# Kernel optimization log

Hardware: AMD Instinct MI355X
Metric: run time of the kernel (lower is better)

## Reference

```python
import jax, jax.numpy as jnp
import numpy as np

BINS = 70
HLO, HHI = -10.0, 10.0
EPS = 1e-5


def _conv_bn(x, w, b, g, be, relu=True):
    # 1x1 Conv1d == channel matmul: x [B,C,N], w [O,C]
    y = jnp.einsum('oc,bcn->bon', w, x) + b[None, :, None]
    # BatchNorm1d in training mode: biased batch stats over (batch, points)
    m = jnp.mean(y, axis=(0, 2))
    v = jnp.var(y, axis=(0, 2))
    y = (y - m[None, :, None]) * jax.lax.rsqrt(v + EPS)[None, :, None]
    y = y * g[None, :, None] + be[None, :, None]
    return jax.nn.relu(y) if relu else y


def _batch_hist(x):
    # Faithful to the torch.histc global-offset hack: one flat histogram with
    # bins*B*F buckets and group offsets of exactly (HHI-HLO); values that fall
    # outside [HLO,HHI] for a given (b,f) leak into neighboring groups, exactly
    # as in the original. Returns argmax bin index per (b,f) as float.
    B, F, N = x.shape
    w = (HHI - HLO) / BINS  # 2/7, and group offset 20 == BINS*w so bins align
    total = BINS * B * F
    grp = jnp.arange(B * F, dtype=jnp.int32).reshape(B, F, 1)
    gidx = jnp.floor((x - HLO) / w).astype(jnp.int32) + BINS * grp
    gidx = jnp.where((gidx >= 0) & (gidx < total), gidx, total)  # drop out-of-range
    counts = jnp.zeros(total + 1, jnp.float32).at[gidx.ravel()].add(1.0)
    h = counts[:total].reshape(B, F, BINS)
    return jnp.argmax(h, axis=-1).astype(jnp.float32)  # [B,F]


def setup_inputs() -> dict:
    key = jax.random.key(0)
    ks = jax.random.split(key, 7)
    d = {
        'x': jax.random.normal(ks[0], (16, 3, 4096), dtype=jnp.float32),
        'w1': jax.random.normal(ks[1], (64, 3), dtype=jnp.float32) * 0.2,
        'b1': jnp.zeros((64,), jnp.float32),
        'g1': jnp.ones((64,), jnp.float32),
        'be1': jnp.zeros((64,), jnp.float32),
        'w2': jax.random.normal(ks[2], (128, 64), dtype=jnp.float32) * 0.1,
        'b2': jnp.zeros((128,), jnp.float32),
        'g2': jnp.ones((128,), jnp.float32),
        'be2': jnp.zeros((128,), jnp.float32),
        'w3': jax.random.normal(ks[3], (1024, 128), dtype=jnp.float32) * 0.08,
        'b3': jnp.zeros((1024,), jnp.float32),
        'g3': jnp.ones((1024,), jnp.float32),
        'be3': jnp.zeros((1024,), jnp.float32),
    }
    return d


def reference(x, w1, b1, g1, be1, w2, b2, g2, be2, w3, b3, g3, be3):
    # PointNetEncoder forward, global_feat=True, robust_type='HS',
    # input/feature transforms disabled (trans, trans_feat are None).
    h = _conv_bn(x, w1, b1, g1, be1, relu=True)    # [B,64,N]
    h = _conv_bn(h, w2, b2, g2, be2, relu=True)    # [B,128,N]
    h = _conv_bn(h, w3, b3, g3, be3, relu=False)   # [B,1024,N]
    feat = _batch_hist(h)                          # [B,1024] mode-bin indices
    return feat
```

## Files before the change

### kernel.cpp

```cpp
#include <hip/hip_runtime.h>

#define EPSF 1e-5f
#define TOTBINS 1146880

typedef _Float16 v8h __attribute__((ext_vector_type(8)));
typedef _Float16 v4h __attribute__((ext_vector_type(4)));
typedef float v4f __attribute__((ext_vector_type(4)));

#define OFF_PARTX   1146880
#define OFF_W1F     1149952
#define OFF_B1F     1150144
#define OFF_PMU1    1150208
#define OFF_M1N     1166592
#define OFF_MU1     1170688
#define OFF_W2H     1170752
#define OFF_W2L     1174848
#define OFF_B2F     1178944
#define OFF_PMU2    1179072
#define OFF_M2N     1211840
#define OFF_MU2     1228224
#define OFF_W3H     1228352
#define OFF_W3L     1293888
#define OFF_B3F     1359424
#define OFF_H1H     1360448
#define OFF_H1L     3457600
#define OFF_H2H     5554752
#define OFF_H2L     9749056

#define GLL(src,dst) __builtin_amdgcn_global_load_lds( \
    (const __attribute__((address_space(1))) void*)(src), \
    (__attribute__((address_space(3))) void*)(dst), 16, 0, 0)

__global__ void k_statsX(const float* __restrict__ x, float* __restrict__ part){
  __shared__ float red[12][256];
  int t = threadIdx.x;
  int s = blockIdx.x*256 + t;
  int b = s >> 12, n = s & 4095;
  const float* xb = x + (size_t)b*12288 + n;
  float x0 = xb[0], x1 = xb[4096], x2 = xb[8192];
  float v[12] = {x0,x1,x2, x0*x0,x0*x1,x0*x2, x1*x1,x1*x2,x2*x2, 0.f,0.f,0.f};
  #pragma unroll
  for(int j=0;j<12;j++) red[j][t]=v[j];
  __syncthreads();
  for(int off=128; off>0; off>>=1){
    if(t<off){
      #pragma unroll
      for(int j=0;j<12;j++) red[j][t]+=red[j][t+off];
    }
    __syncthreads();
  }
  if(t<12) part[blockIdx.x*12+t]=red[t][0];
}

__global__ void k_fold1(const float* __restrict__ part,
                        const float* __restrict__ w1, const float* __restrict__ b1,
                        const float* __restrict__ g1, const float* __restrict__ be1,
                        float* __restrict__ W1f, float* __restrict__ B1f){
  __shared__ double S[12];
  int t=threadIdx.x;
  if(t<12){
    double a=0.0;
    for(int s=0;s<256;s++) a+=(double)part[s*12+t];
    S[t]=a;
  }
  __syncthreads();
  if(t<64){
    double inv = 1.0/65536.0;
    double mu[3]={S[0]*inv,S[1]*inv,S[2]*inv};
    double M[3][3];
    M[0][0]=S[3]*inv; M[0][1]=S[4]*inv; M[0][2]=S[5]*inv;
    M[1][1]=S[6]*inv; M[1][2]=S[7]*inv; M[2][2]=S[8]*inv;
    M[1][0]=M[0][1]; M[2][0]=M[0][2]; M[2][1]=M[1][2];
    double w[3]={(double)w1[t*3],(double)w1[t*3+1],(double)w1[t*3+2]};
    double wm=0.0, q=0.0;
    for(int c=0;c<3;c++){
      wm += w[c]*mu[c];
      for(int d=0;d<3;d++) q += w[c]*w[d]*M[c][d];
    }
    double var = q - wm*wm;
    double m = wm + (double)b1[t];
    double sc = (double)g1[t] / sqrt(var + (double)EPSF);
    for(int c=0;c<3;c++) W1f[t*3+c]=(float)(w[c]*sc);
    B1f[t]=(float)(((double)b1[t]-m)*sc + (double)be1[t]);
  }
}

__global__ void k_layer1(const float* __restrict__ x, const float* __restrict__ W1f,
                         const float* __restrict__ B1f,
                         _Float16* __restrict__ h1h, _Float16* __restrict__ h1l){
  int s = blockIdx.x*256 + threadIdx.x;
  int b = s>>12, n = s&4095;
  const float* xb = x + (size_t)b*12288 + n;
  float x0=xb[0], x1=xb[4096], x2=xb[8192];
  size_t off = ((size_t)((b<<12)+n))<<6;
  #pragma unroll
  for(int q=0;q<8;q++){
    v8h vh, vl;
    #pragma unroll
    for(int e=0;e<8;e++){
      int f=q*8+e;
      float v = fmaf(W1f[f*3+2],x2, fmaf(W1f[f*3+1],x1, fmaf(W1f[f*3],x0, B1f[f])));
      v = v>0.f ? v : 0.f;
      _Float16 hh=(_Float16)v;
      vh[e]=hh;
      vl[e]=(_Float16)(v-(float)hh);
    }
    *(v8h*)(h1h+off+q*8)=vh;
    *(v8h*)(h1l+off+q*8)=vl;
  }
}

__global__ void k_stats1(const _Float16* __restrict__ h1h, const _Float16* __restrict__ h1l,
                         float* __restrict__ partM, float* __restrict__ partMu){
  __shared__ __align__(16) float tl[64][68];
  int t=threadIdx.x, wg=blockIdx.x;
  int s0=wg*256;
  int b=s0>>12, n0=s0&4095;
  int ti=t&15, tj=t>>4;
  float acc[4][4];
  #pragma unroll
  for(int i=0;i<4;i++){
    #pragma unroll
    for(int j=0;j<4;j++) acc[i][j]=0.f;
  }
  float mu=0.f;
  for(int tile=0; tile<4; tile++){
    int nb=n0+tile*64;
    __syncthreads();
    {
      int nr=t>>2, cq=(t&3)<<4;
      const _Float16* ph = h1h + (((size_t)((b<<12)+nb+nr))<<6) + cq;
      const _Float16* pl = h1l + (((size_t)((b<<12)+nb+nr))<<6) + cq;
      #pragma unroll
      for(int q=0;q<2;q++){
        v8h hh=*(const v8h*)(ph+q*8);
        v8h ll=*(const v8h*)(pl+q*8);
        float4 v0=make_float4((float)hh[0]+(float)ll[0],(float)hh[1]+(float)ll[1],
                              (float)hh[2]+(float)ll[2],(float)hh[3]+(float)ll[3]);
        float4 v1=make_float4((float)hh[4]+(float)ll[4],(float)hh[5]+(float)ll[5],
                              (float)hh[6]+(float)ll[6],(float)hh[7]+(float)ll[7]);
        *(float4*)&tl[nr][cq+q*8]   = v0;
        *(float4*)&tl[nr][cq+q*8+4] = v1;
      }
    }
    __syncthreads();
    for(int k=0;k<64;k++){
      float a[4],bb[4];
      #pragma unroll
      for(int i=0;i<4;i++) a[i]=tl[k][i*16+ti];
      #pragma unroll
      for(int j=0;j<4;j++) bb[j]=tl[k][j*16+tj];
      #pragma unroll
      for(int i=0;i<4;i++){
        #pragma unroll
        for(int j=0;j<4;j++) acc[i][j]=fmaf(a[i],bb[j],acc[i][j]);
      }
    }
    if(t<64){
      float ss=0.f;
      for(int k=0;k<64;k++) ss+=tl[k][t];
      mu+=ss;
    }
  }
  #pragma unroll
  for(int i=0;i<4;i++){
    #pragma unroll
    for(int j=0;j<4;j++)
      partM[(size_t)wg*4096+(i*16+ti)*64+(j*16+tj)]=acc[i][j];
  }
  if(t<64) partMu[wg*64+t]=mu;
}

__global__ void k_reduceM1(const float* __restrict__ partM, const float* __restrict__ partMu,
                           float* __restrict__ M1n, float* __restrict__ mu1){
  int e=blockIdx.x*256+threadIdx.x;
  double a=0.0;
  for(int s=0;s<256;s++) a+=(double)partM[(size_t)s*4096+e];
  M1n[e]=(float)(a/65536.0);
  if(e<64){
    double m=0.0;
    for(int s=0;s<256;s++) m+=(double)partMu[s*64+e];
    mu1[e]=(float)(m/65536.0);
  }
}

__global__ void k_fold2(const float* __restrict__ w2, const float* __restrict__ b2,
                        const float* __restrict__ g2, const float* __restrict__ be2,
                        const float* __restrict__ M1n, const float* __restrict__ mu1,
                        _Float16* __restrict__ w2h, _Float16* __restrict__ w2l,
                        float* __restrict__ B2f){
  int f=blockIdx.x, t=threadIdx.x;
  __shared__ float w[64];
  w[t]=w2[f*64+t];
  __syncthreads();
  double tm=0.0;
  for(int c=0;c<64;c++) tm += (double)w[c]*(double)M1n[c*64+t];
  double pv=tm*(double)w[t];
  double pm=(double)w[t]*(double)mu1[t];
  #pragma unroll
  for(int off=32;off>0;off>>=1){
    pv+=__shfl_xor(pv,off,64);
    pm+=__shfl_xor(pm,off,64);
  }
  double var=pv-pm*pm;
  double m=pm+(double)b2[f];
  double sc=(double)g2[f]/sqrt(var+(double)EPSF);
  float Wf=(float)((double)w[t]*sc);
  _Float16 hh=(_Float16)Wf;
  w2h[f*64+t]=hh;
  w2l[f*64+t]=(_Float16)(Wf-(float)hh);
  if(t==0) B2f[f]=(float)(((double)b2[f]-m)*sc+(double)be2[f]);
}

__global__ __launch_bounds__(256,8) void k_layer2(
    const _Float16* __restrict__ h1h, const _Float16* __restrict__ h1l,
    const _Float16* __restrict__ w2h, const _Float16* __restrict__ w2l,
    const float* __restrict__ B2f,
    _Float16* __restrict__ h2h, _Float16* __restrict__ h2l){
  __shared__ __align__(16) _Float16 stage[4][512];
  int t=threadIdx.x, wg=blockIdx.x;
  int wv=t>>6, l=t&63;
  int lrow=l&15, lgrp=l>>4;
  int b=wg>>7;
  int r=wg&127;
  int f0=(r>>6)<<6;
  int n0=(r&63)<<6;
  v8h Ah[2], Al[2];
  {
    const _Float16* ph = w2h + (size_t)(f0 + wv*16 + lrow)*64 + lgrp*8;
    const _Float16* pl = w2l + (size_t)(f0 + wv*16 + lrow)*64 + lgrp*8;
    #pragma unroll
    for(int s=0;s<2;s++){
      Ah[s]=*(const v8h*)(ph+s*32);
      Al[s]=*(const v8h*)(pl+s*32);
    }
  }
  float bias[4];
  #pragma unroll
  for(int rr=0;rr<4;rr++) bias[rr]=B2f[f0+wv*16+lgrp*4+rr];
  int ks=wv>>1, pln=wv&1;
  const _Float16* src = (pln ? h1l : h1h)
      + (((size_t)((b<<12)+n0+lrow))<<6) + ks*32 + lgrp*8;
  _Float16* dst = &stage[wv][0];
  for(int it=0; it<4; it++){
    GLL(src,dst);
    src += 1024;
    __syncthreads();
    v8h Bh[2],Bl[2];
    #pragma unroll
    for(int s=0;s<2;s++){
      Bh[s]=*(const v8h*)&stage[s*2  ][l*8];
      Bl[s]=*(const v8h*)&stage[s*2+1][l*8];
    }
    v4f acc={bias[0],bias[1],bias[2],bias[3]};
    #pragma unroll
    for(int s=0;s<2;s++){
      acc=__builtin_amdgcn_mfma_f32_16x16x32_f16(Ah[s],Bh[s],acc,0,0,0);
      acc=__builtin_amdgcn_mfma_f32_16x16x32_f16(Ah[s],Bl[s],acc,0,0,0);
      acc=__builtin_amdgcn_mfma_f32_16x16x32_f16(Al[s],Bh[s],acc,0,0,0);
    }
    int n=n0+it*16+lrow;
    size_t o=(((size_t)((b<<12)+n))<<7) + f0 + wv*16 + lgrp*4;
    v4h sh, sl4;
    #pragma unroll
    for(int rr=0;rr<4;rr++){
      float v=acc[rr];
      v = v>0.f ? v : 0.f;
      _Float16 hh=(_Float16)v;
      sh[rr]=hh;
      sl4[rr]=(_Float16)(v-(float)hh);
    }
    *(v4h*)(h2h+o)=sh;
    *(v4h*)(h2l+o)=sl4;
    __syncthreads();
  }
}

__global__ void k_stats2(const _Float16* __restrict__ h2h, const _Float16* __restrict__ h2l,
                         float* __restrict__ partM, float* __restrict__ partMu){
  __shared__ __align__(16) float tl[64][132];
  int t=threadIdx.x, wg=blockIdx.x;
  int s0=wg*256;
  int b=s0>>12, n0=s0&4095;
  int ti=t&15, tj=t>>4;
  float acc[8][8];
  #pragma unroll
  for(int i=0;i<8;i++){
    #pragma unroll
    for(int j=0;j<8;j++) acc[i][j]=0.f;
  }
  float mu=0.f;
  for(int tile=0; tile<4; tile++){
    int nb=n0+tile*64;
    __syncthreads();
    {
      int nr=t>>2, cq=(t&3)<<5;
      const _Float16* ph = h2h + ((size_t)((b<<12)+nb+nr))*128 + cq;
      const _Float16* pl = h2l + ((size_t)((b<<12)+nb+nr))*128 + cq;
      #pragma unroll
      for(int q=0;q<4;q++){
        v8h hh=*(const v8h*)(ph+q*8);
        v8h ll=*(const v8h*)(pl+q*8);
        float4 v0=make_float4((float)hh[0]+(float)ll[0],(float)hh[1]+(float)ll[1],
                              (float)hh[2]+(float)ll[2],(float)hh[3]+(float)ll[3]);
        float4 v1=make_float4((float)hh[4]+(float)ll[4],(float)hh[5]+(float)ll[5],
                              (float)hh[6]+(float)ll[6],(float)hh[7]+(float)ll[7]);
        *(float4*)&tl[nr][cq+q*8]   = v0;
        *(float4*)&tl[nr][cq+q*8+4] = v1;
      }
    }
    __syncthreads();
    for(int k=0;k<64;k++){
      float a[8],bb[8];
      #pragma unroll
      for(int i=0;i<8;i++) a[i]=tl[k][i*16+ti];
      #pragma unroll
      for(int j=0;j<8;j++) bb[j]=tl[k][j*16+tj];
      #pragma unroll
      for(int i=0;i<8;i++){
        #pragma unroll
        for(int j=0;j<8;j++) acc[i][j]=fmaf(a[i],bb[j],acc[i][j]);
      }
    }
    if(t<128){
      float s=0.f;
      for(int k=0;k<64;k++) s+=tl[k][t];
      mu+=s;
    }
  }
  #pragma unroll
  for(int i=0;i<8;i++){
    #pragma unroll
    for(int j=0;j<8;j++)
      partM[(size_t)wg*16384+(i*16+ti)*128+(j*16+tj)]=acc[i][j];
  }
  if(t<128) partMu[wg*128+t]=mu;
}

__global__ void k_reduceM2(const float* __restrict__ partM, const float* __restrict__ partMu,
                           float* __restrict__ M2n, float* __restrict__ mu2){
  int e=blockIdx.x*256+threadIdx.x;
  double a=0.0;
  for(int s=0;s<256;s++) a+=(double)partM[(size_t)s*16384+e];
  M2n[e]=(float)(a/65536.0);
  if(e<128){
    double m=0.0;
    for(int s=0;s<256;s++) m+=(double)partMu[s*128+e];
    mu2[e]=(float)(m/65536.0);
  }
}

__global__ void k_fold3(const float* __restrict__ w3, const float* __restrict__ b3,
                        const float* __restrict__ g3, const float* __restrict__ be3,
                        const float* __restrict__ M2n, const float* __restrict__ mu2,
                        _Float16* __restrict__ w3h, _Float16* __restrict__ w3l,
                        float* __restrict__ B3f){
  int f=blockIdx.x, t=threadIdx.x;
  __shared__ float w[128];
  __shared__ double rv[2], rm[2];
  w[t]=w3[f*128+t];
  __syncthreads();
  double tm=0.0;
  for(int c=0;c<128;c++) tm += (double)w[c]*(double)M2n[c*128+t];
  double pv=tm*(double)w[t];
  double pm=(double)w[t]*(double)mu2[t];
  #pragma unroll
  for(int off=32;off>0;off>>=1){
    pv+=__shfl_xor(pv,off,64);
    pm+=__shfl_xor(pm,off,64);
  }
  if((t&63)==0){ rv[t>>6]=pv; rm[t>>6]=pm; }
  __syncthreads();
  double pmt=rm[0]+rm[1];
  double var=(rv[0]+rv[1]) - pmt*pmt;
  double m=pmt + (double)b3[f];
  double sc=(double)g3[f]/sqrt(var+(double)EPSF);
  float Wf=(float)((double)w[t]*sc);
  _Float16 hh=(_Float16)Wf;
  w3h[f*128+t]=hh;
  w3l[f*128+t]=(_Float16)(Wf-(float)hh);
  if(t==0) B3f[f]=(float)(((double)b3[f]-m)*sc+(double)be3[f]);
}

__global__ __launch_bounds__(256,4) void k_gemm3_hist(
    const _Float16* __restrict__ h2h, const _Float16* __restrict__ h2l,
    const _Float16* __restrict__ w3h, const _Float16* __restrict__ w3l,
    const float* __restrict__ B3f, unsigned int* __restrict__ hist){
  __shared__ __align__(16) _Float16 stage[2][8][512];
  __shared__ unsigned int lh[4480];
  int t=threadIdx.x, wg=blockIdx.x;
  int wv=t>>6, l=t&63;
  int lrow=l&15, lgrp=l>>4;
  int b=wg>>6;
  int r=wg&63;
  int f0=(r>>3)<<7;
  int sl=r&7;
  int base=70*((b<<10)+f0);
  for(int i=t;i<4480;i+=256) lh[i]=0u;

  v8h Ah[2][4], Al[2][4];
  #pragma unroll
  for(int T=0;T<2;T++){
    const _Float16* ph = w3h + (size_t)(f0 + wv*32 + T*16 + lrow)*128 + lgrp*8;
    const _Float16* pl = w3l + (size_t)(f0 + wv*32 + T*16 + lrow)*128 + lgrp*8;
    #pragma unroll
    for(int s=0;s<4;s++){
      Ah[T][s]=*(const v8h*)(ph+s*32);
      Al[T][s]=*(const v8h*)(pl+s*32);
    }
  }
  float bias[2][4]; int base70[2][4];
  #pragma unroll
  for(int T=0;T<2;T++){
    #pragma unroll
    for(int rr=0;rr<4;rr++){
      int fl_=wv*32+T*16+lgrp*4+rr;
      bias[T][rr]=B3f[f0+fl_];
      base70[T][rr]=fl_*70;
    }
  }
  const float wbin=(10.0f-(-10.0f))/70.0f;
  const float inv_w=1.0f/wbin;
  const float off_w=10.0f*inv_w;

  const _Float16* pH = h2h + ((size_t)((b<<12)+sl*512+lrow))*128 + wv*32 + lgrp*8;
  const _Float16* pL = h2l + ((size_t)((b<<12)+sl*512+lrow))*128 + wv*32 + lgrp*8;

#define ISSUE(B_) { GLL(pH,&stage[B_][wv*2][0]); GLL(pL,&stage[B_][wv*2+1][0]); \
                    pH+=2048; pL+=2048; }
#define COMPUTE(B_) { \
    v4f acc0={bias[0][0],bias[0][1],bias[0][2],bias[0][3]}; \
    v4f acc1={bias[1][0],bias[1][1],bias[1][2],bias[1][3]}; \
    _Pragma("unroll") \
    for(int s=0;s<4;s++){ \
      v8h Bh=*(const v8h*)&stage[B_][s*2  ][l*8]; \
      v8h Bl=*(const v8h*)&stage[B_][s*2+1][l*8]; \
      acc0=__builtin_amdgcn_mfma_f32_16x16x32_f16(Ah[0][s],Bh,acc0,0,0,0); \
      acc0=__builtin_amdgcn_mfma_f32_16x16x32_f16(Ah[0][s],Bl,acc0,0,0,0); \
      acc0=__builtin_amdgcn_mfma_f32_16x16x32_f16(Al[0][s],Bh,acc0,0,0,0); \
      acc1=__builtin_amdgcn_mfma_f32_16x16x32_f16(Ah[1][s],Bh,acc1,0,0,0); \
      acc1=__builtin_amdgcn_mfma_f32_16x16x32_f16(Ah[1][s],Bl,acc1,0,0,0); \
      acc1=__builtin_amdgcn_mfma_f32_16x16x32_f16(Al[1][s],Bh,acc1,0,0,0); \
    } \
    _Pragma("unroll") \
    for(int T=0;T<2;T++){ \
      v4f accT = T ? acc1 : acc0; \
      _Pragma("unroll") \
      for(int rr=0;rr<4;rr++){ \
        float q=fmaf(accT[rr],inv_w,off_w); \
        if(q>-2.0e9f && q<2.0e9f){ \
          int bin=(int)floorf(q); \
          int loc=base70[T][rr]+bin; \
          if((unsigned)loc<8960u){ \
            atomicAdd(&lh[loc>>1], 1u<<((loc&1)<<4)); \
          }else{ \
            int g=base+loc; \
            if(g>=0 && g<TOTBINS) atomicAdd(&hist[g],1u); \
          } \
        } \
      } \
    } }

  ISSUE(0);
  __syncthreads();
  for(int ii=0;ii<16;ii++){
    ISSUE(1);
    COMPUTE(0);
    __syncthreads();
    if(ii<15) ISSUE(0);
    COMPUTE(1);
    __syncthreads();
  }
#undef ISSUE
#undef COMPUTE
  for(int i=t;i<4480;i+=256){
    unsigned int c=lh[i];
    if(c&0xFFFFu) atomicAdd(&hist[base+2*i],   c&0xFFFFu);
    if(c>>16)     atomicAdd(&hist[base+2*i+1], c>>16);
  }
}

__global__ void k_argmax(const unsigned int* __restrict__ hist, float* __restrict__ out){
  int g = blockIdx.x*256 + threadIdx.x;
  const unsigned int* h = hist + (size_t)g*70;
  unsigned int best=h[0]; int arg=0;
  for(int k=1;k<70;k++){
    unsigned int c=h[k];
    if(c>best){ best=c; arg=k; }
  }
  out[g]=(float)arg;
}

extern "C" void kernel_launch(void* const* d_in, const int* in_sizes, int n_in,
                              void* d_out, int out_size, void* d_ws, size_t ws_size,
                              hipStream_t stream){
  const float* x  =(const float*)d_in[0];
  const float* w1 =(const float*)d_in[1];
  const float* b1 =(const float*)d_in[2];
  const float* g1 =(const float*)d_in[3];
  const float* be1=(const float*)d_in[4];
  const float* w2 =(const float*)d_in[5];
  const float* b2 =(const float*)d_in[6];
  const float* g2 =(const float*)d_in[7];
  const float* be2=(const float*)d_in[8];
  const float* w3 =(const float*)d_in[9];
  const float* b3 =(const float*)d_in[10];
  const float* g3 =(const float*)d_in[11];
  const float* be3=(const float*)d_in[12];

  float* ws=(float*)d_ws;
  unsigned int* hist=(unsigned int*)ws;
  float* partX = ws+OFF_PARTX;
  float* W1f   = ws+OFF_W1F;
  float* B1f   = ws+OFF_B1F;
  float* pMu1  = ws+OFF_PMU1;
  float* M1n   = ws+OFF_M1N;
  float* mu1   = ws+OFF_MU1;
  _Float16* w2h=(_Float16*)(ws+OFF_W2H);
  _Float16* w2l=(_Float16*)(ws+OFF_W2L);
  float* B2f   = ws+OFF_B2F;
  float* pMu2  = ws+OFF_PMU2;
  float* M2n   = ws+OFF_M2N;
  float* mu2   = ws+OFF_MU2;
  _Float16* w3h=(_Float16*)(ws+OFF_W3H);
  _Float16* w3l=(_Float16*)(ws+OFF_W3L);
  float* B3f   = ws+OFF_B3F;
  _Float16* h1h=(_Float16*)(ws+OFF_H1H);
  _Float16* h1l=(_Float16*)(ws+OFF_H1L);
  _Float16* h2h=(_Float16*)(ws+OFF_H2H);
  _Float16* h2l=(_Float16*)(ws+OFF_H2L);
  float* partM1=(float*)(ws+OFF_H2H);
  float* partM2=(float*)(ws+OFF_H1H);

  hipMemsetAsync(hist, 0, (size_t)TOTBINS*sizeof(unsigned int), stream);

  k_statsX  <<<256,256,0,stream>>>(x, partX);
  k_fold1   <<<1,  256,0,stream>>>(partX,w1,b1,g1,be1,W1f,B1f);
  k_layer1  <<<256,256,0,stream>>>(x,W1f,B1f,h1h,h1l);
  k_stats1  <<<256,256,0,stream>>>(h1h,h1l,partM1,pMu1);
  k_reduceM1<<<16, 256,0,stream>>>(partM1,pMu1,M1n,mu1);
  k_fold2   <<<128, 64,0,stream>>>(w2,b2,g2,be2,M1n,mu1,w2h,w2l,B2f);
  k_layer2  <<<2048,256,0,stream>>>(h1h,h1l,w2h,w2l,B2f,h2h,h2l);
  k_stats2  <<<256,256,0,stream>>>(h2h,h2l,partM2,pMu2);
  k_reduceM2<<<64, 256,0,stream>>>(partM2,pMu2,M2n,mu2);
  k_fold3   <<<1024,128,0,stream>>>(w3,b3,g3,be3,M2n,mu2,w3h,w3l,B3f);
  k_gemm3_hist<<<1024,256,0,stream>>>(h2h,h2l,w3h,w3l,B3f,hist);
  k_argmax  <<<64, 256,0,stream>>>(hist,(float*)d_out);
}
```

Baseline: 251.5 us.

## Privatize layer-3 LDS histogram into four 8-bit copies; double-buffer layer-2 staging

The fused GEMM3+histogram kernel now keeps four private LDS histogram copies selected by lane&3. Each copy packs four 8-bit counters per word instead of two 16-bit counters, which should cut LDS atomic contention. The copies are summed when flushed to global memory. The fused kernel's launch bounds drop from 4 to 3 blocks per CU to make room for the larger LDS footprint. Layer 2 gets a double-buffered stage so the next global-to-LDS load overlaps the current MFMA compute. The NaN/huge-value range check before the float-to-int conversion is removed, and the 8-bit counters depend on per-copy counts staying at or below 255.

```diff
diff --git a/kernel.cpp b/kernel.cpp
--- a/kernel.cpp
+++ b/kernel.cpp
@@ -217,7 +217,7 @@
     const _Float16* __restrict__ w2h, const _Float16* __restrict__ w2l,
     const float* __restrict__ B2f,
     _Float16* __restrict__ h2h, _Float16* __restrict__ h2l){
-  __shared__ __align__(16) _Float16 stage[4][512];
+  __shared__ __align__(16) _Float16 stage[2][4][512];
   int t=threadIdx.x, wg=blockIdx.x;
   int wv=t>>6, l=t&63;
   int lrow=l&15, lgrp=l>>4;
@@ -241,39 +241,44 @@
   int ks=wv>>1, pln=wv&1;
   const _Float16* src = (pln ? h1l : h1h)
       + (((size_t)((b<<12)+n0+lrow))<<6) + ks*32 + lgrp*8;
-  _Float16* dst = &stage[wv][0];
-  for(int it=0; it<4; it++){
-    GLL(src,dst);
-    src += 1024;
-    __syncthreads();
-    v8h Bh[2],Bl[2];
-    #pragma unroll
-    for(int s=0;s<2;s++){
-      Bh[s]=*(const v8h*)&stage[s*2  ][l*8];
-      Bl[s]=*(const v8h*)&stage[s*2+1][l*8];
-    }
-    v4f acc={bias[0],bias[1],bias[2],bias[3]};
-    #pragma unroll
-    for(int s=0;s<2;s++){
-      acc=__builtin_amdgcn_mfma_f32_16x16x32_f16(Ah[s],Bh[s],acc,0,0,0);
-      acc=__builtin_amdgcn_mfma_f32_16x16x32_f16(Ah[s],Bl[s],acc,0,0,0);
-      acc=__builtin_amdgcn_mfma_f32_16x16x32_f16(Al[s],Bh[s],acc,0,0,0);
-    }
-    int n=n0+it*16+lrow;
-    size_t o=(((size_t)((b<<12)+n))<<7) + f0 + wv*16 + lgrp*4;
-    v4h sh, sl4;
-    #pragma unroll
-    for(int rr=0;rr<4;rr++){
-      float v=acc[rr];
-      v = v>0.f ? v : 0.f;
-      _Float16 hh=(_Float16)v;
-      sh[rr]=hh;
-      sl4[rr]=(_Float16)(v-(float)hh);
-    }
-    *(v4h*)(h2h+o)=sh;
-    *(v4h*)(h2l+o)=sl4;
-    __syncthreads();
-  }
+
+#define L2ISSUE(B_) { GLL(src,&stage[B_][wv][0]); src += 1024; }
+#define L2COMPUTE(B_,IT) { \
+    v8h Bh[2],Bl[2]; \
+    _Pragma("unroll") \
+    for(int s=0;s<2;s++){ \
+      Bh[s]=*(const v8h*)&stage[B_][s*2  ][l*8]; \
+      Bl[s]=*(const v8h*)&stage[B_][s*2+1][l*8]; \
+    } \
+    v4f acc={bias[0],bias[1],bias[2],bias[3]}; \
+    _Pragma("unroll") \
+    for(int s=0;s<2;s++){ \
+      acc=__builtin_amdgcn_mfma_f32_16x16x32_f16(Ah[s],Bh[s],acc,0,0,0); \
+      acc=__builtin_amdgcn_mfma_f32_16x16x32_f16(Ah[s],Bl[s],acc,0,0,0); \
+      acc=__builtin_amdgcn_mfma_f32_16x16x32_f16(Al[s],Bh[s],acc,0,0,0); \
+    } \
+    int n=n0+(IT)*16+lrow; \
+    size_t o=(((size_t)((b<<12)+n))<<7) + f0 + wv*16 + lgrp*4; \
+    v4h sh, sl4; \
+    _Pragma("unroll") \
+    for(int rr=0;rr<4;rr++){ \
+      float v=acc[rr]; \
+      v = v>0.f ? v : 0.f; \
+      _Float16 hh=(_Float16)v; \
+      sh[rr]=hh; \
+      sl4[rr]=(_Float16)(v-(float)hh); \
+    } \
+    *(v4h*)(h2h+o)=sh; \
+    *(v4h*)(h2l+o)=sl4; }
+
+  L2ISSUE(0);
+  __syncthreads();
+  L2ISSUE(1); L2COMPUTE(0,0); __syncthreads();
+  L2ISSUE(0); L2COMPUTE(1,1); __syncthreads();
+  L2ISSUE(1); L2COMPUTE(0,2); __syncthreads();
+              L2COMPUTE(1,3);
+#undef L2ISSUE
+#undef L2COMPUTE
 }
 
 __global__ void k_stats2(const _Float16* __restrict__ h2h, const _Float16* __restrict__ h2l,
@@ -382,12 +387,12 @@
   if(t==0) B3f[f]=(float)(((double)b3[f]-m)*sc+(double)be3[f]);
 }
 
-__global__ __launch_bounds__(256,4) void k_gemm3_hist(
+__global__ __launch_bounds__(256,3) void k_gemm3_hist(
     const _Float16* __restrict__ h2h, const _Float16* __restrict__ h2l,
     const _Float16* __restrict__ w3h, const _Float16* __restrict__ w3l,
     const float* __restrict__ B3f, unsigned int* __restrict__ hist){
   __shared__ __align__(16) _Float16 stage[2][8][512];
-  __shared__ unsigned int lh[4480];
+  __shared__ unsigned int lh[4*2248];
   int t=threadIdx.x, wg=blockIdx.x;
   int wv=t>>6, l=t&63;
   int lrow=l&15, lgrp=l>>4;
@@ -396,7 +401,8 @@
   int f0=(r>>3)<<7;
   int sl=r&7;
   int base=70*((b<<10)+f0);
-  for(int i=t;i<4480;i+=256) lh[i]=0u;
+  for(int i=t;i<4*2248;i+=256) lh[i]=0u;
+  unsigned int* lhp = lh + (l&3)*2248;
 
   v8h Ah[2][4], Al[2][4];
   #pragma unroll
@@ -448,15 +454,13 @@
       _Pragma("unroll") \
       for(int rr=0;rr<4;rr++){ \
         float q=fmaf(accT[rr],inv_w,off_w); \
-        if(q>-2.0e9f && q<2.0e9f){ \
-          int bin=(int)floorf(q); \
-          int loc=base70[T][rr]+bin; \
-          if((unsigned)loc<8960u){ \
-            atomicAdd(&lh[loc>>1], 1u<<((loc&1)<<4)); \
-          }else{ \
-            int g=base+loc; \
-            if(g>=0 && g<TOTBINS) atomicAdd(&hist[g],1u); \
-          } \
+        int bin=(int)floorf(q); \
+        int loc=base70[T][rr]+bin; \
+        if((unsigned)loc<8960u){ \
+          atomicAdd(&lhp[loc>>2], 1u<<((loc&3)<<3)); \
+        }else{ \
+          int g=base+loc; \
+          if(g>=0 && g<TOTBINS) atomicAdd(&hist[g],1u); \
         } \
       } \
     } }
@@ -473,10 +477,18 @@
   }
 #undef ISSUE
 #undef COMPUTE
-  for(int i=t;i<4480;i+=256){
-    unsigned int c=lh[i];
-    if(c&0xFFFFu) atomicAdd(&hist[base+2*i],   c&0xFFFFu);
-    if(c>>16)     atomicAdd(&hist[base+2*i+1], c>>16);
+  for(int i=t;i<2240;i+=256){
+    unsigned c0=0,c1=0,c2=0,c3=0;
+    #pragma unroll
+    for(int cp=0;cp<4;cp++){
+      unsigned w=lh[cp*2248+i];
+      c0+=w&0xffu; c1+=(w>>8)&0xffu; c2+=(w>>16)&0xffu; c3+=w>>24;
+    }
+    int bb=base+4*i;
+    if(c0) atomicAdd(&hist[bb  ],c0);
+    if(c1) atomicAdd(&hist[bb+1],c1);
+    if(c2) atomicAdd(&hist[bb+2],c2);
+    if(c3) atomicAdd(&hist[bb+3],c3);
   }
 }
 
```

Result: slower. 284.6 us (+13.1%).
